# Kernel tuning notes

Hardware: AMD Instinct MI355X
Metric: run time of the kernel (lower is better)

The kernel has to match this reference:

```python
import jax, jax.numpy as jnp
import numpy as np

NUM_HEADS = 16
DIM = 1024
HEAD_DIM = DIM // NUM_HEADS
SCALE = DIM ** (-0.5)  # note: module scales by dim_out**-0.5, not head_dim**-0.5
ROPE_THETA = 10000.0


def _rope_cos_sin(seq_len, head_dim, dtype):
    # lucidrains default: freqs = 1/theta^(arange(0,d,2)/d), interleaved-repeat to d
    inv_freq = 1.0 / (ROPE_THETA ** (np.arange(0, head_dim, 2, dtype=np.float32) / head_dim))
    t = np.arange(seq_len, dtype=np.float32)
    freqs = np.einsum('i,j->ij', t, inv_freq)            # [T, d/2]
    freqs = np.repeat(freqs, 2, axis=-1)                  # [T, d] interleaved repeat
    return jnp.asarray(np.cos(freqs), dtype), jnp.asarray(np.sin(freqs), dtype)


def _rotate_half(x):
    # interleaved pairs: (x1, x2) -> (-x2, x1)
    x1 = x[..., ::2]
    x2 = x[..., 1::2]
    return jnp.stack([-x2, x1], axis=-1).reshape(x.shape)


def _apply_rope(x, cos, sin):
    # x: [B, H, T, d]; cos/sin: [T, d]
    return x * cos + _rotate_half(x) * sin


def setup_inputs() -> dict:
    key = jax.random.key(0)
    ks = jax.random.split(key, 6)
    B, T = 4, 2048
    s = DIM ** -0.5
    return {
        'x':  jax.random.normal(ks[0], (B, T, DIM), jnp.float32),
        'h':  32,
        'w':  64,
        'Wq': jax.random.normal(ks[1], (DIM, DIM), jnp.float32) * s,
        'Wk': jax.random.normal(ks[2], (DIM, DIM), jnp.float32) * s,
        'Wv': jax.random.normal(ks[3], (DIM, DIM), jnp.float32) * s,
        'Wp': jax.random.normal(ks[4], (DIM, DIM), jnp.float32) * s,
        'bp': jax.random.normal(ks[5], (DIM,), jnp.float32) * 0.01,
    }


def reference(x, h, w, Wq, Wk, Wv, Wp, bp):
    B, T, _ = x.shape
    split = lambda y: y.reshape(B, T, NUM_HEADS, HEAD_DIM).transpose(0, 2, 1, 3)  # b h t d
    q = split(x @ Wq)
    k = split(x @ Wk)
    v = split(x @ Wv)
    cos, sin = _rope_cos_sin(T, HEAD_DIM, x.dtype)
    q = _apply_rope(q, cos, sin)
    k = _apply_rope(k, cos, sin)
    attn = jax.nn.softmax(jnp.einsum('bhld,bhtd->bhlt', q, k) * SCALE, axis=-1)
    out = jnp.einsum('bhlt,bhtd->bhld', attn, v)
    out = out.transpose(0, 2, 1, 3).reshape(B, T, DIM)  # b t (h d)
    return out @ Wp + bp
```

## Files before the change

### kernel.cpp

```cpp
#include <hip/hip_runtime.h>

typedef unsigned short u16;
typedef unsigned int u32;
typedef __attribute__((ext_vector_type(8))) short short8;
typedef __attribute__((ext_vector_type(4))) short short4v;
typedef __attribute__((ext_vector_type(4))) float f32x4;
typedef __attribute__((ext_vector_type(16))) float f32x16;

__device__ __forceinline__ u16 f2bf(float f) {
  u32 u = __float_as_uint(f);
  u = (u + 0x7fffu + ((u >> 16) & 1u)) >> 16;
  return (u16)u;
}
__device__ __forceinline__ float bf2f(u16 h) {
  return __uint_as_float(((u32)h) << 16);
}
__device__ __forceinline__ void glds16(const u16* g, u16* l) {
  __builtin_amdgcn_global_load_lds(
      (const __attribute__((address_space(1))) void*)g,
      (__attribute__((address_space(3))) void*)l, 16, 0, 0);
}

__global__ __launch_bounds__(256) void rope_tab_k(u32* __restrict__ cst) {
  int idx = blockIdx.x * 256 + threadIdx.x;
  int t = idx >> 5, i = idx & 31;
  float inv = powf(10000.0f, -(float)i / 32.0f);
  float ang = (float)t * inv;
  float s, c;
  sincosf(ang, &s, &c);
  cst[idx] = (u32)f2bf(c) | ((u32)f2bf(s) << 16);
}

__global__ __launch_bounds__(256) void cvt_x_k(const float* __restrict__ x,
                                               u16* __restrict__ xb) {
  int i = blockIdx.x * 256 + threadIdx.x;
  int e = i * 8;
  float4 a = *(const float4*)(x + e);
  float4 b = *(const float4*)(x + e + 4);
  short8 o;
  o[0] = (short)f2bf(a.x); o[1] = (short)f2bf(a.y);
  o[2] = (short)f2bf(a.z); o[3] = (short)f2bf(a.w);
  o[4] = (short)f2bf(b.x); o[5] = (short)f2bf(b.y);
  o[6] = (short)f2bf(b.z); o[7] = (short)f2bf(b.w);
  *(short8*)(xb + e) = o;
}

__global__ __launch_bounds__(256) void wtrans_k(const float* __restrict__ W0,
                                                const float* __restrict__ W1,
                                                const float* __restrict__ W2,
                                                const float* __restrict__ W3,
                                                u16* __restrict__ wt) {
  __shared__ float tl[64][65];
  const float* W = (blockIdx.z == 0) ? W0 : (blockIdx.z == 1) ? W1
                  : (blockIdx.z == 2) ? W2 : W3;
  u16* out = wt + (size_t)blockIdx.z * 1024 * 1024;
  int k0 = blockIdx.x * 64, n0 = blockIdx.y * 64;
  int tid = threadIdx.x;
  int rr = tid >> 4, cc4 = (tid & 15) * 4;
#pragma unroll
  for (int p = 0; p < 4; ++p) {
    int r = rr + p * 16;
    float4 v = *(const float4*)(W + (size_t)(k0 + r) * 1024 + n0 + cc4);
    tl[r][cc4] = v.x; tl[r][cc4 + 1] = v.y; tl[r][cc4 + 2] = v.z; tl[r][cc4 + 3] = v.w;
  }
  __syncthreads();
#pragma unroll
  for (int p = 0; p < 4; ++p) {
    int rn = rr + p * 16;
    short4v o;
    o[0] = (short)f2bf(tl[cc4][rn]);     o[1] = (short)f2bf(tl[cc4 + 1][rn]);
    o[2] = (short)f2bf(tl[cc4 + 2][rn]); o[3] = (short)f2bf(tl[cc4 + 3][rn]);
    *(short4v*)(out + (size_t)(n0 + rn) * 1024 + k0 + cc4) = o;
  }
}

__global__ __launch_bounds__(256) void gemm_qkv_k(const u16* __restrict__ xb,
                                                  const u16* __restrict__ wt,
                                                  const u32* __restrict__ cst,
                                                  u16* __restrict__ Qb,
                                                  u16* __restrict__ Kb,
                                                  u16* __restrict__ Vt) {
  __shared__ __align__(16) u16 Ash[128][32];
  __shared__ __align__(16) u16 Bsh[128][32];
  __shared__ __align__(16) u32 csl[4096];
  int tid = threadIdx.x;
  int lane = tid & 63, w = tid >> 6;
  int wr = w >> 1, wc = w & 1;
  int l15 = lane & 15, g = lane >> 4;

  int row0 = blockIdx.x * 128;
  int ncol0 = blockIdx.y * 128;
  int which = blockIdx.y >> 3;

  if (which < 2) {
    const u16* src = (const u16*)(cst + (size_t)(row0 & 2047) * 32);
#pragma unroll
    for (int p = 0; p < 4; ++p)
      glds16(src + p * 2048 + tid * 8, (u16*)csl + p * 2048 + tid * 8);
  }

  f32x4 zero = {0.f, 0.f, 0.f, 0.f};
  f32x4 acc[4][4];
#pragma unroll
  for (int m = 0; m < 4; ++m)
#pragma unroll
    for (int n = 0; n < 4; ++n) acc[m][n] = zero;

  int aRow = tid >> 2, aK = (tid & 3) * 8;
  const u16* aSrc0 = xb + (size_t)(row0 + aRow) * 1024 + aK;
  const u16* aSrc1 = xb + (size_t)(row0 + 64 + aRow) * 1024 + aK;
  const u16* bSrc0 = wt + (size_t)(ncol0 + aRow) * 1024 + aK;
  const u16* bSrc1 = wt + (size_t)(ncol0 + 64 + aRow) * 1024 + aK;
  u16* ldsA0 = &Ash[0][0] + tid * 8;
  u16* ldsA1 = &Ash[0][0] + 2048 + tid * 8;
  u16* ldsB0 = &Bsh[0][0] + tid * 8;
  u16* ldsB1 = &Bsh[0][0] + 2048 + tid * 8;

  for (int kt = 0; kt < 32; ++kt) {
    __syncthreads();
    glds16(aSrc0, ldsA0); glds16(aSrc1, ldsA1);
    glds16(bSrc0, ldsB0); glds16(bSrc1, ldsB1);
    aSrc0 += 32; aSrc1 += 32; bSrc0 += 32; bSrc1 += 32;
    __syncthreads();
    short8 af[4], bfr[4];
#pragma unroll
    for (int m = 0; m < 4; ++m) af[m] = *(const short8*)&Ash[wr * 64 + m * 16 + l15][g * 8];
#pragma unroll
    for (int n = 0; n < 4; ++n) bfr[n] = *(const short8*)&Bsh[wc * 64 + n * 16 + l15][g * 8];
#pragma unroll
    for (int m = 0; m < 4; ++m)
#pragma unroll
      for (int n = 0; n < 4; ++n)
        acc[m][n] = __builtin_amdgcn_mfma_f32_16x16x32_bf16(af[m], bfr[n], acc[m][n], 0, 0, 0);
  }

  int c0 = ncol0 + wc * 64;
  int rb = row0 + wr * 64;
  u32 sgnbit = (l15 & 1) ? 0u : 0x80000000u;
  float qscale = (which == 0) ? 0.03125f : 1.0f;
#pragma unroll
  for (int m = 0; m < 4; ++m) {
    int r = rb + m * 16 + g * 4;
    int bb = r >> 11, t = r & 2047;
    int rowin = wr * 64 + m * 16 + g * 4;
#pragma unroll
    for (int n = 0; n < 4; ++n) {
      int c = c0 + n * 16 + l15;
      int hh = (c & 1023) >> 6, d = c & 63;
      if (which == 2) {
        short4v o;
        o[0] = (short)f2bf(acc[m][n][0]); o[1] = (short)f2bf(acc[m][n][1]);
        o[2] = (short)f2bf(acc[m][n][2]); o[3] = (short)f2bf(acc[m][n][3]);
        *(short4v*)(Vt + ((size_t)((bb * 16 + hh) * 64 + d)) * 2048 + t) = o;
      } else {
        u16* dst = (which == 0 ? Qb : Kb) + ((size_t)((bb * 16 + hh) * 2048 + t)) * 64 + d;
        int ci = (d >> 1);
#pragma unroll
        for (int j = 0; j < 4; ++j) {
          float v = acc[m][n][j];
          float p = __shfl_xor(v, 1);
          u32 cs = csl[(rowin + j) * 32 + ci];
          float c_ = __uint_as_float(cs << 16);
          float s_ = __uint_as_float(cs & 0xffff0000u);
          float ps = __uint_as_float(__float_as_uint(p * s_) ^ sgnbit);
          float o = fmaf(v, c_, ps) * qscale;
          dst[j * 64] = f2bf(o);
        }
      }
    }
  }
}

__global__ __launch_bounds__(256) void attn_k(const u16* __restrict__ Q,
                                              const u16* __restrict__ K,
                                              const u16* __restrict__ Vt,
                                              u16* __restrict__ O) {
  __shared__ __align__(16) u16 KVs[2][2][4096];
  int bid = blockIdx.x;
  int head = (bid & 7) + ((bid >> 7) << 3);
  int qt = (bid >> 3) & 15;
  int bb = head >> 4, hh = head & 15;
  const u16* Qh = Q + (size_t)head * 131072;
  const u16* Kh = K + (size_t)head * 131072;
  const u16* Vh = Vt + (size_t)head * 131072;
  int tid = threadIdx.x, lane = tid & 63, w = tid >> 6;
  int l31 = lane & 31, hi = lane >> 5;
  int t0 = qt * 128 + w * 32;

  int srow = tid >> 3;
  int scol = ((tid & 7) ^ (srow & 7)) * 8;

  short8 qf[4];
#pragma unroll
  for (int ks = 0; ks < 4; ++ks)
    qf[ks] = *(const short8*)(Qh + (size_t)(t0 + l31) * 64 + ks * 16 + hi * 8);

  const u16* lds0 = &KVs[0][0][0];
  const u16* rpp[4];
#pragma unroll
  for (int j = 0; j < 4; ++j)
    rpp[j] = lds0 + l31 * 64 + ((((j * 2 + hi) ^ (lane & 7))) << 3);

  f32x16 zz;
#pragma unroll
  for (int i = 0; i < 16; ++i) zz[i] = 0.f;
  f32x16 oa0 = zz, oa1 = zz, oa2 = zz;
  short8 ones8 = {16256, 16256, 16256, 16256, 16256, 16256, 16256, 16256};

  const u16* kp = Kh + srow * 64 + scol;
  const u16* vp = Vh + srow * 2048 + scol;
  u16* sK = &KVs[0][0][0] + tid * 8;
  u16* sV = &KVs[0][1][0] + tid * 8;

#define STAGE_AT(BO) do {                                                      \
    glds16(kp,         sK + (BO));                                             \
    glds16(kp + 2048,  sK + (BO) + 2048);                                      \
    glds16(vp,         sV + (BO));                                             \
    glds16(vp + 65536, sV + (BO) + 2048);                                      \
    kp += 4096; vp += 64;                                                      \
  } while (0)

#define ATT_TILE(OB) do {                                                      \
    _Pragma("unroll")                                                          \
    for (int bl = 0; bl < 2; ++bl) {                                           \
      f32x16 pb = zz;                                                          \
      __builtin_amdgcn_s_setprio(1);                                           \
      _Pragma("unroll")                                                        \
      for (int ks = 0; ks < 4; ++ks) {                                         \
        short8 kf = *(const short8*)(rpp[ks] + (OB) + bl * 2048);              \
        pb = __builtin_amdgcn_mfma_f32_32x32x16_bf16(kf, qf[ks], pb, 0, 0, 0); \
      }                                                                        \
      __builtin_amdgcn_s_setprio(0);                                           \
      _Pragma("unroll")                                                        \
      for (int r = 0; r < 16; ++r) pb[r] = __expf(pb[r]);                      \
      u32 pk8[8];                                                              \
      _Pragma("unroll")                                                        \
      for (int j = 0; j < 8; ++j)                                              \
        asm("v_cvt_pk_bf16_f32 %0, %1, %2"                                     \
            : "=v"(pk8[j]) : "v"(pb[2 * j]), "v"(pb[2 * j + 1]));              \
      _Pragma("unroll")                                                        \
      for (int kb = 0; kb < 2; ++kb) {                                         \
        u32 w0 = pk8[4 * kb + 0], w2 = pk8[4 * kb + 2];                        \
        u32 w1 = pk8[4 * kb + 1], w3 = pk8[4 * kb + 3];                        \
        asm("v_permlane32_swap_b32 %0, %1" : "+v"(w0), "+v"(w2));              \
        asm("v_permlane32_swap_b32 %0, %1" : "+v"(w1), "+v"(w3));              \
        union { u32 u[4]; short8 s; } pu;                                      \
        pu.u[0] = w0; pu.u[1] = w1; pu.u[2] = w2; pu.u[3] = w3;                \
        const int kss = bl * 2 + kb;                                           \
        short8 vf0 = *(const short8*)(rpp[kss] + (OB) + 4096);                 \
        short8 vf1 = *(const short8*)(rpp[kss] + (OB) + 4096 + 2048);          \
        __builtin_amdgcn_s_setprio(1);                                         \
        oa0 = __builtin_amdgcn_mfma_f32_32x32x16_bf16(pu.s, vf0, oa0, 0,0,0);  \
        oa1 = __builtin_amdgcn_mfma_f32_32x32x16_bf16(pu.s, vf1, oa1, 0,0,0);  \
        oa2 = __builtin_amdgcn_mfma_f32_32x32x16_bf16(pu.s, ones8, oa2, 0,0,0);\
        __builtin_amdgcn_s_setprio(0);                                         \
      }                                                                        \
    }                                                                          \
  } while (0)

  STAGE_AT(0);
  for (int it = 0; it < 16; ++it) {
    STAGE_AT(8192);
    asm volatile("s_waitcnt vmcnt(4)\ns_barrier" ::: "memory");
    ATT_TILE(0);
    asm volatile("s_barrier" ::: "memory");
    if (it < 15) {
      STAGE_AT(0);
      asm volatile("s_waitcnt vmcnt(4)\ns_barrier" ::: "memory");
    } else {
      asm volatile("s_waitcnt vmcnt(0)\ns_barrier" ::: "memory");
    }
    ATT_TILE(8192);
    asm volatile("s_barrier" ::: "memory");
  }
#undef STAGE_AT
#undef ATT_TILE

  size_t obase = (size_t)(bb * 2048 + t0) * 1024 + hh * 64 + l31;
#pragma unroll
  for (int r = 0; r < 16; ++r) {
    int qr = (r & 3) + ((r >> 2) << 3) + (hi << 2);
    float ir = 1.0f / oa2[r];
    O[obase + (size_t)qr * 1024]      = f2bf(oa0[r] * ir);
    O[obase + (size_t)qr * 1024 + 32] = f2bf(oa1[r] * ir);
  }
}

__global__ __launch_bounds__(256) void gemm_out_k(const u16* __restrict__ Ob,
                                                  const u16* __restrict__ wt,
                                                  const float* __restrict__ bp,
                                                  float* __restrict__ out) {
  __shared__ __align__(16) u16 Ash[128][32];
  __shared__ __align__(16) u16 Bsh[128][32];
  int tid = threadIdx.x;
  int lane = tid & 63, w = tid >> 6;
  int wr = w >> 1, wc = w & 1;
  int l15 = lane & 15, g = lane >> 4;
  int row0 = blockIdx.x * 128;
  int ncol0 = blockIdx.y * 128;

  f32x4 zero = {0.f, 0.f, 0.f, 0.f};
  f32x4 acc[4][4];
#pragma unroll
  for (int m = 0; m < 4; ++m)
#pragma unroll
    for (int n = 0; n < 4; ++n) acc[m][n] = zero;

  int aRow = tid >> 2, aK = (tid & 3) * 8;
  const u16* aSrc0 = Ob + (size_t)(row0 + aRow) * 1024 + aK;
  const u16* aSrc1 = Ob + (size_t)(row0 + 64 + aRow) * 1024 + aK;
  const u16* bSrc0 = wt + (size_t)(ncol0 + aRow) * 1024 + aK;
  const u16* bSrc1 = wt + (size_t)(ncol0 + 64 + aRow) * 1024 + aK;
  u16* ldsA0 = &Ash[0][0] + tid * 8;
  u16* ldsA1 = &Ash[0][0] + 2048 + tid * 8;
  u16* ldsB0 = &Bsh[0][0] + tid * 8;
  u16* ldsB1 = &Bsh[0][0] + 2048 + tid * 8;

  for (int kt = 0; kt < 32; ++kt) {
    __syncthreads();
    glds16(aSrc0, ldsA0); glds16(aSrc1, ldsA1);
    glds16(bSrc0, ldsB0); glds16(bSrc1, ldsB1);
    aSrc0 += 32; aSrc1 += 32; bSrc0 += 32; bSrc1 += 32;
    __syncthreads();
    short8 af[4], bfr[4];
#pragma unroll
    for (int m = 0; m < 4; ++m) af[m] = *(const short8*)&Ash[wr * 64 + m * 16 + l15][g * 8];
#pragma unroll
    for (int n = 0; n < 4; ++n) bfr[n] = *(const short8*)&Bsh[wc * 64 + n * 16 + l15][g * 8];
#pragma unroll
    for (int m = 0; m < 4; ++m)
#pragma unroll
      for (int n = 0; n < 4; ++n)
        acc[m][n] = __builtin_amdgcn_mfma_f32_16x16x32_bf16(af[m], bfr[n], acc[m][n], 0, 0, 0);
  }

  int c0 = ncol0 + wc * 64;
  int rb = row0 + wr * 64;
  float bn[4];
#pragma unroll
  for (int n = 0; n < 4; ++n) bn[n] = bp[c0 + n * 16 + l15];
#pragma unroll
  for (int m = 0; m < 4; ++m) {
    int r = rb + m * 16 + g * 4;
#pragma unroll
    for (int n = 0; n < 4; ++n) {
      int c = c0 + n * 16 + l15;
      out[(size_t)(r + 0) * 1024 + c] = acc[m][n][0] + bn[n];
      out[(size_t)(r + 1) * 1024 + c] = acc[m][n][1] + bn[n];
      out[(size_t)(r + 2) * 1024 + c] = acc[m][n][2] + bn[n];
      out[(size_t)(r + 3) * 1024 + c] = acc[m][n][3] + bn[n];
    }
  }
}

extern "C" void kernel_launch(void* const* d_in, const int* in_sizes, int n_in,
                              void* d_out, int out_size, void* d_ws, size_t ws_size,
                              hipStream_t stream) {
  const float* x  = (const float*)d_in[0];
  const float* Wq = (const float*)d_in[3];
  const float* Wk = (const float*)d_in[4];
  const float* Wv = (const float*)d_in[5];
  const float* Wp = (const float*)d_in[6];
  const float* bp = (const float*)d_in[7];
  float* out = (float*)d_out;

  char* ws = (char*)d_ws;
  u16* xb   = (u16*)(ws);
  u16* wt   = (u16*)(ws + 16777216);
  u16* Qb   = (u16*)(ws + 25165824);
  u16* Kb   = (u16*)(ws + 41943040);
  u16* Vt   = (u16*)(ws + 58720256);
  u16* Ob   = (u16*)(ws + 75497472);
  u32* cst  = (u32*)(ws + 92274688);

  rope_tab_k<<<256, 256, 0, stream>>>(cst);
  cvt_x_k<<<4096, 256, 0, stream>>>(x, xb);
  dim3 tg(16, 16, 4);
  wtrans_k<<<tg, 256, 0, stream>>>(Wq, Wk, Wv, Wp, wt);
  dim3 g1(64, 24);
  gemm_qkv_k<<<g1, 256, 0, stream>>>(xb, wt, cst, Qb, Kb, Vt);
  attn_k<<<1024, 256, 0, stream>>>(Qb, Kb, Vt, Ob);
  dim3 g2(64, 8);
  gemm_out_k<<<g2, 256, 0, stream>>>(Ob, wt + (size_t)3 * 1024 * 1024, bp, out);
}
```

Before: 210.9 us.

## Merge prep kernels, move Q RoPE into attention, simplify attention pipeline waits

Combines the x conversion, RoPE table and weight transpose kernels into one launch to cut launch overhead. Q RoPE and scaling move from the QKV GEMM epilogue into the attention kernel's Q fragment load, so Q blocks in the GEMM no longer stage the cos/sin table. The attention loop's partial vmcnt waits are replaced with full waits plus barriers after each tile. This may reduce load/compute overlap.

```diff
diff --git a/kernel.cpp b/kernel.cpp
--- a/kernel.cpp
+++ b/kernel.cpp
@@ -21,56 +21,56 @@
       (__attribute__((address_space(3))) void*)l, 16, 0, 0);
 }
 
-__global__ __launch_bounds__(256) void rope_tab_k(u32* __restrict__ cst) {
-  int idx = blockIdx.x * 256 + threadIdx.x;
-  int t = idx >> 5, i = idx & 31;
-  float inv = powf(10000.0f, -(float)i / 32.0f);
-  float ang = (float)t * inv;
-  float s, c;
-  sincosf(ang, &s, &c);
-  cst[idx] = (u32)f2bf(c) | ((u32)f2bf(s) << 16);
-}
-
-__global__ __launch_bounds__(256) void cvt_x_k(const float* __restrict__ x,
-                                               u16* __restrict__ xb) {
-  int i = blockIdx.x * 256 + threadIdx.x;
-  int e = i * 8;
-  float4 a = *(const float4*)(x + e);
-  float4 b = *(const float4*)(x + e + 4);
-  short8 o;
-  o[0] = (short)f2bf(a.x); o[1] = (short)f2bf(a.y);
-  o[2] = (short)f2bf(a.z); o[3] = (short)f2bf(a.w);
-  o[4] = (short)f2bf(b.x); o[5] = (short)f2bf(b.y);
-  o[6] = (short)f2bf(b.z); o[7] = (short)f2bf(b.w);
-  *(short8*)(xb + e) = o;
-}
-
-__global__ __launch_bounds__(256) void wtrans_k(const float* __restrict__ W0,
-                                                const float* __restrict__ W1,
-                                                const float* __restrict__ W2,
-                                                const float* __restrict__ W3,
-                                                u16* __restrict__ wt) {
+__global__ __launch_bounds__(256) void prep_k(const float* __restrict__ x,
+                                              u16* __restrict__ xb,
+                                              const float* __restrict__ W0,
+                                              const float* __restrict__ W1,
+                                              const float* __restrict__ W2,
+                                              const float* __restrict__ W3,
+                                              u16* __restrict__ wt,
+                                              u32* __restrict__ cst) {
   __shared__ float tl[64][65];
-  const float* W = (blockIdx.z == 0) ? W0 : (blockIdx.z == 1) ? W1
-                  : (blockIdx.z == 2) ? W2 : W3;
-  u16* out = wt + (size_t)blockIdx.z * 1024 * 1024;
-  int k0 = blockIdx.x * 64, n0 = blockIdx.y * 64;
+  int bid = blockIdx.x;
   int tid = threadIdx.x;
-  int rr = tid >> 4, cc4 = (tid & 15) * 4;
-#pragma unroll
-  for (int p = 0; p < 4; ++p) {
-    int r = rr + p * 16;
-    float4 v = *(const float4*)(W + (size_t)(k0 + r) * 1024 + n0 + cc4);
-    tl[r][cc4] = v.x; tl[r][cc4 + 1] = v.y; tl[r][cc4 + 2] = v.z; tl[r][cc4 + 3] = v.w;
-  }
-  __syncthreads();
-#pragma unroll
-  for (int p = 0; p < 4; ++p) {
-    int rn = rr + p * 16;
-    short4v o;
-    o[0] = (short)f2bf(tl[cc4][rn]);     o[1] = (short)f2bf(tl[cc4 + 1][rn]);
-    o[2] = (short)f2bf(tl[cc4 + 2][rn]); o[3] = (short)f2bf(tl[cc4 + 3][rn]);
-    *(short4v*)(out + (size_t)(n0 + rn) * 1024 + k0 + cc4) = o;
+  if (bid < 4096) {
+    int e = (bid * 256 + tid) * 8;
+    float4 a = *(const float4*)(x + e);
+    float4 b = *(const float4*)(x + e + 4);
+    short8 o;
+    o[0] = (short)f2bf(a.x); o[1] = (short)f2bf(a.y);
+    o[2] = (short)f2bf(a.z); o[3] = (short)f2bf(a.w);
+    o[4] = (short)f2bf(b.x); o[5] = (short)f2bf(b.y);
+    o[6] = (short)f2bf(b.z); o[7] = (short)f2bf(b.w);
+    *(short8*)(xb + e) = o;
+  } else if (bid < 4352) {
+    int idx = (bid - 4096) * 256 + tid;
+    int t = idx >> 5, i = idx & 31;
+    float inv = powf(10000.0f, -(float)i / 32.0f);
+    float ang = (float)t * inv;
+    float s, c;
+    sincosf(ang, &s, &c);
+    cst[idx] = (u32)f2bf(c) | ((u32)f2bf(s) << 16);
+  } else {
+    int blk = bid - 4352;
+    int k0 = (blk & 15) * 64, n0 = ((blk >> 4) & 15) * 64, wz = blk >> 8;
+    const float* W = (wz == 0) ? W0 : (wz == 1) ? W1 : (wz == 2) ? W2 : W3;
+    u16* out = wt + (size_t)wz * 1024 * 1024;
+    int rr = tid >> 4, cc4 = (tid & 15) * 4;
+#pragma unroll
+    for (int p = 0; p < 4; ++p) {
+      int r = rr + p * 16;
+      float4 v = *(const float4*)(W + (size_t)(k0 + r) * 1024 + n0 + cc4);
+      tl[r][cc4] = v.x; tl[r][cc4 + 1] = v.y; tl[r][cc4 + 2] = v.z; tl[r][cc4 + 3] = v.w;
+    }
+    __syncthreads();
+#pragma unroll
+    for (int p = 0; p < 4; ++p) {
+      int rn = rr + p * 16;
+      short4v o;
+      o[0] = (short)f2bf(tl[cc4][rn]);     o[1] = (short)f2bf(tl[cc4 + 1][rn]);
+      o[2] = (short)f2bf(tl[cc4 + 2][rn]); o[3] = (short)f2bf(tl[cc4 + 3][rn]);
+      *(short4v*)(out + (size_t)(n0 + rn) * 1024 + k0 + cc4) = o;
+    }
   }
 }
 
@@ -92,7 +92,7 @@
   int ncol0 = blockIdx.y * 128;
   int which = blockIdx.y >> 3;
 
-  if (which < 2) {
+  if (which == 1) {
     const u16* src = (const u16*)(cst + (size_t)(row0 & 2047) * 32);
 #pragma unroll
     for (int p = 0; p < 4; ++p)
@@ -137,7 +137,6 @@
   int c0 = ncol0 + wc * 64;
   int rb = row0 + wr * 64;
   u32 sgnbit = (l15 & 1) ? 0u : 0x80000000u;
-  float qscale = (which == 0) ? 0.03125f : 1.0f;
 #pragma unroll
   for (int m = 0; m < 4; ++m) {
     int r = rb + m * 16 + g * 4;
@@ -152,8 +151,14 @@
         o[0] = (short)f2bf(acc[m][n][0]); o[1] = (short)f2bf(acc[m][n][1]);
         o[2] = (short)f2bf(acc[m][n][2]); o[3] = (short)f2bf(acc[m][n][3]);
         *(short4v*)(Vt + ((size_t)((bb * 16 + hh) * 64 + d)) * 2048 + t) = o;
+      } else if (which == 0) {
+        u16* dst = Qb + ((size_t)((bb * 16 + hh) * 2048 + t)) * 64 + d;
+        dst[0]   = f2bf(acc[m][n][0]);
+        dst[64]  = f2bf(acc[m][n][1]);
+        dst[128] = f2bf(acc[m][n][2]);
+        dst[192] = f2bf(acc[m][n][3]);
       } else {
-        u16* dst = (which == 0 ? Qb : Kb) + ((size_t)((bb * 16 + hh) * 2048 + t)) * 64 + d;
+        u16* dst = Kb + ((size_t)((bb * 16 + hh) * 2048 + t)) * 64 + d;
         int ci = (d >> 1);
 #pragma unroll
         for (int j = 0; j < 4; ++j) {
@@ -163,8 +168,7 @@
           float c_ = __uint_as_float(cs << 16);
           float s_ = __uint_as_float(cs & 0xffff0000u);
           float ps = __uint_as_float(__float_as_uint(p * s_) ^ sgnbit);
-          float o = fmaf(v, c_, ps) * qscale;
-          dst[j * 64] = f2bf(o);
+          dst[j * 64] = f2bf(fmaf(v, c_, ps));
         }
       }
     }
@@ -174,6 +178,7 @@
 __global__ __launch_bounds__(256) void attn_k(const u16* __restrict__ Q,
                                               const u16* __restrict__ K,
                                               const u16* __restrict__ Vt,
+                                              const u32* __restrict__ cst,
                                               u16* __restrict__ O) {
   __shared__ __align__(16) u16 KVs[2][2][4096];
   int bid = blockIdx.x;
@@ -191,9 +196,25 @@
   int scol = ((tid & 7) ^ (srow & 7)) * 8;
 
   short8 qf[4];
-#pragma unroll
-  for (int ks = 0; ks < 4; ++ks)
-    qf[ks] = *(const short8*)(Qh + (size_t)(t0 + l31) * 64 + ks * 16 + hi * 8);
+  {
+    const uint4* cr = (const uint4*)(cst + (size_t)(t0 + l31) * 32);
+#pragma unroll
+    for (int ks = 0; ks < 4; ++ks) {
+      short8 q = *(const short8*)(Qh + (size_t)(t0 + l31) * 64 + ks * 16 + hi * 8);
+      uint4 cs4 = cr[ks * 2 + hi];
+      const u32* csp = (const u32*)&cs4;
+      short8 o;
+#pragma unroll
+      for (int p = 0; p < 4; ++p) {
+        u32 cs = csp[p];
+        float c_ = bf2f((u16)cs), s_ = bf2f((u16)(cs >> 16));
+        float a = bf2f((u16)q[2 * p]), b = bf2f((u16)q[2 * p + 1]);
+        o[2 * p]     = (short)f2bf((a * c_ - b * s_) * 0.03125f);
+        o[2 * p + 1] = (short)f2bf((b * c_ + a * s_) * 0.03125f);
+      }
+      qf[ks] = o;
+    }
+  }
 
   const u16* lds0 = &KVs[0][0][0];
   const u16* rpp[4];
@@ -219,6 +240,8 @@
     glds16(vp + 65536, sV + (BO) + 2048);                                      \
     kp += 4096; vp += 64;                                                      \
   } while (0)
+
+#define WAIT_BAR asm volatile("s_waitcnt vmcnt(0)\ns_barrier" ::: "memory")
 
 #define ATT_TILE(OB) do {                                                      \
     _Pragma("unroll")                                                          \
@@ -259,22 +282,20 @@
   } while (0)
 
   STAGE_AT(0);
+  WAIT_BAR;
   for (int it = 0; it < 16; ++it) {
     STAGE_AT(8192);
-    asm volatile("s_waitcnt vmcnt(4)\ns_barrier" ::: "memory");
     ATT_TILE(0);
-    asm volatile("s_barrier" ::: "memory");
+    WAIT_BAR;
     if (it < 15) {
       STAGE_AT(0);
-      asm volatile("s_waitcnt vmcnt(4)\ns_barrier" ::: "memory");
-    } else {
-      asm volatile("s_waitcnt vmcnt(0)\ns_barrier" ::: "memory");
     }
     ATT_TILE(8192);
-    asm volatile("s_barrier" ::: "memory");
+    WAIT_BAR;
   }
 #undef STAGE_AT
 #undef ATT_TILE
+#undef WAIT_BAR
 
   size_t obase = (size_t)(bb * 2048 + t0) * 1024 + hh * 64 + l31;
 #pragma unroll
@@ -373,13 +394,10 @@
   u16* Ob   = (u16*)(ws + 75497472);
   u32* cst  = (u32*)(ws + 92274688);
 
-  rope_tab_k<<<256, 256, 0, stream>>>(cst);
-  cvt_x_k<<<4096, 256, 0, stream>>>(x, xb);
-  dim3 tg(16, 16, 4);
-  wtrans_k<<<tg, 256, 0, stream>>>(Wq, Wk, Wv, Wp, wt);
+  prep_k<<<5376, 256, 0, stream>>>(x, xb, Wq, Wk, Wv, Wp, wt, cst);
   dim3 g1(64, 24);
   gemm_qkv_k<<<g1, 256, 0, stream>>>(xb, wt, cst, Qb, Kb, Vt);
-  attn_k<<<1024, 256, 0, stream>>>(Qb, Kb, Vt, Ob);
+  attn_k<<<1024, 256, 0, stream>>>(Qb, Kb, Vt, cst, Ob);
   dim3 g2(64, 8);
   gemm_out_k<<<g2, 256, 0, stream>>>(Ob, wt + (size_t)3 * 1024 * 1024, bp, out);
 }
```

Result: faster. 206.3 us (-2.2%).
